# Kernel tuning notes

Measured on AMD Instinct MI355X. Metric: run time of the kernel, lower is better.

Reference implementation:

```python
import jax, jax.numpy as jnp
import numpy as np

N_NODES = 100
F_IN = 65536
C_OUT = 60
ACTION_DIM = 100
N_EDGES = 2000


def setup_inputs() -> dict:
    key = jax.random.key(0)
    ks = jax.random.split(key, 16)
    s = 0.02
    return {
        "substrate_features": jax.random.normal(ks[0], (1, N_NODES, F_IN), jnp.float32),
        "edge_index": jax.random.randint(ks[1], (2, N_EDGES), 0, N_NODES, dtype=jnp.int32),
        "v_cpu_demand_t": jax.random.uniform(ks[2], (1,), jnp.float32),
        "v_bw_demand_t": jax.random.uniform(ks[3], (1,), jnp.float32),
        "num_pending_v_nodes_t": jax.random.uniform(ks[4], (1,), jnp.float32),
        "actor_w": jax.random.normal(ks[5], (3, F_IN, C_OUT), jnp.float32) * s,
        "actor_b": jax.random.normal(ks[6], (C_OUT,), jnp.float32) * s,
        "critic_w": jax.random.normal(ks[7], (3, F_IN, C_OUT), jnp.float32) * s,
        "critic_b": jax.random.normal(ks[8], (C_OUT,), jnp.float32) * s,
        "actor_fc_w": jax.random.normal(ks[9], (N_NODES * C_OUT + 3, ACTION_DIM), jnp.float32) * s,
        "actor_fc_b": jax.random.normal(ks[10], (ACTION_DIM,), jnp.float32) * s,
        "critic_fc_w": jax.random.normal(ks[11], (N_NODES * C_OUT + 3, 1), jnp.float32) * s,
        "critic_fc_b": jax.random.normal(ks[12], (1,), jnp.float32) * s,
    }


def cheb_conv(x, edge_index, W, b):
    # ChebConv, K=3, sym normalization, lambda_max=2 (PyG defaults).
    # With lambda_max=2 the scaled Laplacian is L_hat = -D^{-1/2} A D^{-1/2}
    # (diagonal becomes 0 after the -1 self-loop shift).
    # x: [1, N, F]; edge_index: [2, E]; W: [3, F, C]; b: [C]
    src, dst = edge_index[0], edge_index[1]
    n = x.shape[1]
    deg = jax.ops.segment_sum(jnp.ones(src.shape[0], x.dtype), src, num_segments=n)
    dis = jnp.where(deg > 0, jax.lax.rsqrt(jnp.where(deg > 0, deg, 1.0)), 0.0)
    norm = -(dis[src] * dis[dst])  # [E], L_hat off-diagonal entries
    x2 = x[0]  # [N, F]

    def prop(z):  # z: [N, F] -> L_hat @ z via gather/scatter over edges
        return jax.ops.segment_sum(z[src] * norm[:, None], dst, num_segments=n)

    Tx0 = x2
    Tx1 = prop(Tx0)
    Tx2 = 2.0 * prop(Tx1) - Tx0
    out = Tx0 @ W[0] + Tx1 @ W[1] + Tx2 @ W[2] + b  # [N, C]
    return out[None]  # [1, N, C]


def reference(substrate_features, edge_index, v_cpu_demand_t, v_bw_demand_t,
              num_pending_v_nodes_t, actor_w, actor_b, critic_w, critic_b,
              actor_fc_w, actor_fc_b, critic_fc_w, critic_fc_b):
    emb_a = jnp.tanh(cheb_conv(substrate_features, edge_index, actor_w, actor_b))
    emb_a = emb_a.reshape(1, -1)  # [1, N*60]
    emb_c = jnp.tanh(cheb_conv(substrate_features, edge_index, critic_w, critic_b))
    emb_c = emb_c.reshape(1, -1)
    extras = [v_cpu_demand_t[None], v_bw_demand_t[None], num_pending_v_nodes_t[None]]  # each [1,1]
    state_a = jnp.concatenate([emb_a] + extras, axis=1)  # [1, 6003]
    state_c = jnp.concatenate([emb_c] + extras, axis=1)
    logits = state_a @ actor_fc_w + actor_fc_b  # [1, action_dim]
    values = state_c @ critic_fc_w + critic_fc_b  # [1, 1]
    return (logits, values)
```

## Files before the change

kernel.cpp:

```cpp
#include <hip/hip_runtime.h>
#include <stdint.h>

#define F_IN 65536
#define NN 100
#define CO 60
#define G2 256
#define KC (F_IN/G2)
#define BK 64
#define NIT (KC/BK)
#define AST 72
#define BTILE (BK*CO)
#define BQ3 (3*BTILE/4)

typedef short v8s __attribute__((ext_vector_type(8)));
typedef float v4f __attribute__((ext_vector_type(4)));

__device__ __forceinline__ unsigned int f2bf(float x){
  unsigned int u = __float_as_uint(x);
  u += 0x7fffu + ((u>>16)&1u);
  return u>>16;
}

__device__ __forceinline__ v4f mfma16(v8s a, v8s b, v4f c){
  return __builtin_amdgcn_mfma_f32_16x16x32_bf16(a,b,c,0,0,0);
}

__global__ __launch_bounds__(256,2)
void k_gemm(const float* __restrict__ x, const float* __restrict__ aw,
            const float* __restrict__ cw, float* __restrict__ dst, int partial){
  const int bid  = blockIdx.x;
  const int xcd  = bid & 7, slot = bid >> 3;
  const int net  = slot & 1;
  const int s    = xcd*32 + (slot >> 1);
  const int k0   = s*KC;
  const int tid  = threadIdx.x;
  const int wave = tid>>6, lane = tid&63, quad = lane>>4, nl = lane&15;
  const int c0   = wave*16;
  const int ccl  = min(c0+nl, CO-1);

  const float* Wn = net ? cw : aw;

  __shared__ __align__(16) unsigned short Al[2][112*AST];
  __shared__ __align__(16) unsigned short Bl[2][3*BTILE];

  unsigned int boff[12];
  #pragma unroll
  for(int p=0;p<12;++p){
    int li = min(p*256 + tid, BQ3-1);
    int gp = li/960, fp = li - gp*960;
    boff[p] = (unsigned int)((size_t)gp*F_IN*CO + (size_t)fp*4)*4u;
  }
  const char* bbase0 = (const char*)(Wn + (size_t)k0*CO);

  float4 ra[7];
  float4 rbv[12];
  #pragma unroll
  for(int p=0;p<7;++p){
    int lin = p*256 + tid, row = lin>>4, q = lin&15;
    int rcl = min(row, NN-1);
    ra[p] = *(const float4*)(x + (size_t)rcl*F_IN + k0 + q*4);
  }
  #pragma unroll
  for(int p=0;p<12;++p) rbv[p] = *(const float4*)(bbase0 + boff[p]);

  v4f acc[3][7];
  #pragma unroll
  for(int g=0;g<3;++g)
    #pragma unroll
    for(int i=0;i<7;++i){ v4f z={0.f,0.f,0.f,0.f}; acc[g][i]=z; }

  for(int it=0; it<NIT; ++it){
    unsigned short* buf  = Al[it&1];
    unsigned short* bbuf = Bl[it&1];
    #pragma unroll
    for(int p=0;p<7;++p){
      int lin = p*256 + tid, row = lin>>4, q = lin&15;
      uint2 w;
      w.x = f2bf(ra[p].x) | (f2bf(ra[p].y)<<16);
      w.y = f2bf(ra[p].z) | (f2bf(ra[p].w)<<16);
      *(uint2*)(buf + row*AST + q*4) = w;
    }
    #pragma unroll
    for(int p=0;p<12;++p){
      int lin = p*256 + tid;
      if(lin < BQ3){
        uint2 w;
        w.x = f2bf(rbv[p].x) | (f2bf(rbv[p].y)<<16);
        w.y = f2bf(rbv[p].z) | (f2bf(rbv[p].w)<<16);
        *(uint2*)(bbuf + lin*4) = w;
      }
    }
    __syncthreads();
    if(it+1 < NIT){
      const int kb = k0 + (it+1)*BK;
      #pragma unroll
      for(int p=0;p<7;++p){
        int lin = p*256 + tid, row = lin>>4, q = lin&15;
        int rcl = min(row, NN-1);
        ra[p] = *(const float4*)(x + (size_t)rcl*F_IN + kb + q*4);
      }
      const char* bb2 = bbase0 + (size_t)(it+1)*BK*CO*4;
      #pragma unroll
      for(int p=0;p<12;++p) rbv[p] = *(const float4*)(bb2 + boff[p]);
    }
    __builtin_amdgcn_sched_barrier(0);
    v8s fB0[3], fB1[3];
    #pragma unroll
    for(int g=0;g<3;++g){
      const unsigned short* bb = bbuf + g*BTILE + quad*8*CO + ccl;
      #pragma unroll
      for(int j=0;j<8;++j){
        fB0[g][j] = (short)bb[j*CO];
        fB1[g][j] = (short)bb[32*CO + j*CO];
      }
    }
    #pragma unroll
    for(int mt=0; mt<7; ++mt){
      const unsigned short* arow = buf + (mt*16+nl)*AST + quad*8;
      v8s a0 = *(const v8s*)(arow);
      v8s a1 = *(const v8s*)(arow+32);
      #pragma unroll
      for(int g=0;g<3;++g){
        acc[g][mt] = mfma16(a0, fB0[g], acc[g][mt]);
        acc[g][mt] = mfma16(a1, fB1[g], acc[g][mt]);
      }
    }
  }

  const int c = c0 + nl;
  if(c < CO){
    #pragma unroll
    for(int g=0;g<3;++g){
      if(partial){
        float* pd = dst + ((size_t)(net*3+g)*G2 + s)*(NN*CO);
        #pragma unroll
        for(int mt=0;mt<7;++mt){
          #pragma unroll
          for(int i=0;i<4;++i){
            int m = mt*16 + quad*4 + i;
            if(m < NN) pd[m*CO + c] = acc[g][mt][i];
          }
        }
      } else {
        float* pd = dst + (size_t)(net*3+g)*(NN*CO);
        #pragma unroll
        for(int mt=0;mt<7;++mt){
          #pragma unroll
          for(int i=0;i<4;++i){
            int m = mt*16 + quad*4 + i;
            if(m < NN) atomicAdd(pd + m*CO + c, acc[g][mt][i]);
          }
        }
      }
    }
  }
}

__global__ void k_reduce(const float* __restrict__ P, float* __restrict__ Y){
  int o = blockIdx.x*256 + threadIdx.x;
  if(o >= 6*NN*CO) return;
  int gg = o/(NN*CO), r = o - gg*(NN*CO);
  const float* p = P + (size_t)gg*G2*(NN*CO) + (size_t)blockIdx.y*16*(NN*CO) + r;
  float a0=0.f,a1=0.f,a2=0.f,a3=0.f;
  #pragma unroll
  for(int s4=0;s4<16;s4+=4){
    a0 += p[(size_t)(s4  )*(NN*CO)];
    a1 += p[(size_t)(s4+1)*(NN*CO)];
    a2 += p[(size_t)(s4+2)*(NN*CO)];
    a3 += p[(size_t)(s4+3)*(NN*CO)];
  }
  atomicAdd(&Y[o], (a0+a1)+(a2+a3));
}

__global__ void k_cheb(const float* __restrict__ Y, const int* __restrict__ ei,
                       const float* __restrict__ ab, const float* __restrict__ cb,
                       float* __restrict__ emb, float* __restrict__ out){
  const int net = blockIdx.x / CO;
  const int c   = blockIdx.x % CO;
  const int t   = threadIdx.x;
  __shared__ float L[NN][NN+1];
  __shared__ float dis[NN];
  __shared__ int   deg[NN];
  __shared__ float y0[NN], y1[NN], y2[NN], zu[NN];

  if(blockIdx.x==0 && t<101) out[t] = 0.f;

  for(int i=t;i<NN*(NN+1);i+=128) ((float*)L)[i]=0.f;
  if(t<NN) deg[t]=0;
  __syncthreads();
  for(int e=t;e<2000;e+=128) atomicAdd(&deg[ei[e]],1);
  __syncthreads();
  if(t<NN) dis[t] = deg[t]>0 ? rsqrtf((float)deg[t]) : 0.f;
  __syncthreads();
  for(int e=t;e<2000;e+=128){
    int ss = ei[e], d = ei[2000+e];
    atomicAdd(&L[d][ss], -dis[ss]*dis[d]);
  }
  if(t<NN){
    const float* yb = Y + (size_t)net*3*NN*CO + t*CO + c;
    y0[t]=yb[0]; y1[t]=yb[NN*CO]; y2[t]=yb[2*NN*CO];
  }
  __syncthreads();
  if(t<NN){
    float sv=0.f;
    #pragma unroll 4
    for(int j=0;j<NN;++j) sv += L[t][j]*y2[j];
    zu[t] = y1[t] + 2.f*sv;
  }
  __syncthreads();
  if(t<NN){
    float sv=0.f;
    #pragma unroll 4
    for(int j=0;j<NN;++j) sv += L[t][j]*zu[j];
    float b = (net==0) ? ab[c] : cb[c];
    emb[net*NN*CO + t*CO + c] = tanhf(y0[t] - y2[t] + sv + b);
  }
}

#define FCB 50
__global__ void k_fc(const float* __restrict__ emb, const float* __restrict__ afw,
                     const float* __restrict__ afb, const float* __restrict__ cfw,
                     const float* __restrict__ cfb, const float* __restrict__ s0,
                     const float* __restrict__ s1, const float* __restrict__ s2,
                     float* __restrict__ out){
  const int b = blockIdx.x;
  const int t = threadIdx.x;
  if(b < FCB){
    const int jj = t & 127, half = t >> 7;
    if(jj < 100){
      const int i0 = b*120 + half*60;
      const float* w = afw + (size_t)i0*100 + jj;
      const float* e = emb + i0;
      float p0=0.f,p1=0.f,p2=0.f,p3=0.f;
      #pragma unroll 3
      for(int i=0;i<60;i+=4){
        p0 += e[i  ]*w[(size_t)(i  )*100];
        p1 += e[i+1]*w[(size_t)(i+1)*100];
        p2 += e[i+2]*w[(size_t)(i+2)*100];
        p3 += e[i+3]*w[(size_t)(i+3)*100];
      }
      atomicAdd(&out[jj], (p0+p1)+(p2+p3));
    }
  } else {
    float p = 0.f;
    const float* e = emb + 6000;
    for(int i=t;i<6000;i+=256) p += e[i]*cfw[i];
    #pragma unroll
    for(int o=32;o>0;o>>=1) p += __shfl_down(p,o,64);
    __shared__ float red[4];
    if((t&63)==0) red[t>>6]=p;
    __syncthreads();
    if(t==0){
      float tot = red[0]+red[1]+red[2]+red[3];
      out[100] = tot + s0[0]*cfw[6000] + s1[0]*cfw[6001] + s2[0]*cfw[6002] + cfb[0];
    }
    if(t<100){
      atomicAdd(&out[t], afb[t] + s0[0]*afw[600000+t] + s1[0]*afw[600100+t] + s2[0]*afw[600200+t]);
    }
  }
}

extern "C" void kernel_launch(void* const* d_in, const int* in_sizes, int n_in,
                              void* d_out, int out_size, void* d_ws, size_t ws_size,
                              hipStream_t stream){
  const float* x   = (const float*)d_in[0];
  const int*   ei  = (const int*)d_in[1];
  const float* s0  = (const float*)d_in[2];
  const float* s1  = (const float*)d_in[3];
  const float* s2  = (const float*)d_in[4];
  const float* aw  = (const float*)d_in[5];
  const float* ab  = (const float*)d_in[6];
  const float* cw  = (const float*)d_in[7];
  const float* cb  = (const float*)d_in[8];
  const float* afw = (const float*)d_in[9];
  const float* afb = (const float*)d_in[10];
  const float* cfw = (const float*)d_in[11];
  const float* cfb = (const float*)d_in[12];
  float* out = (float*)d_out;

  float* Y   = (float*)d_ws;
  float* emb = Y + 6*NN*CO;
  float* P   = emb + 2*NN*CO;
  const size_t need = (size_t)(6*NN*CO + 2*NN*CO)*4 + (size_t)6*G2*NN*CO*4;
  const int partial = (ws_size >= need) ? 1 : 0;

  hipMemsetAsync(Y, 0, 6*NN*CO*sizeof(float), stream);

  if(partial){
    k_gemm<<<dim3(512), 256, 0, stream>>>(x, aw, cw, P, 1);
    k_reduce<<<dim3((6*NN*CO+255)/256, 16), 256, 0, stream>>>(P, Y);
  } else {
    k_gemm<<<dim3(512), 256, 0, stream>>>(x, aw, cw, Y, 0);
  }
  k_cheb<<<120, 128, 0, stream>>>(Y, ei, ab, cb, emb, out);
  k_fc<<<FCB+1, 256, 0, stream>>>(emb, afw, afb, cfw, cfb, s0, s1, s2, out);
}
```

Baseline: 238.6 us.

## Load GEMM tiles directly into LDS via global_load_lds and convert to bf16 at read time

```diff
diff --git a/kernel.cpp b/kernel.cpp
--- a/kernel.cpp
+++ b/kernel.cpp
@@ -6,23 +6,32 @@
 #define CO 60
 #define G2 256
 #define KC (F_IN/G2)
-#define BK 64
+#define BK 32
 #define NIT (KC/BK)
-#define AST 72
-#define BTILE (BK*CO)
-#define BQ3 (3*BTILE/4)
+#define ABUF 4096
+#define BBUF 5760
 
 typedef short v8s __attribute__((ext_vector_type(8)));
 typedef float v4f __attribute__((ext_vector_type(4)));
 
-__device__ __forceinline__ unsigned int f2bf(float x){
-  unsigned int u = __float_as_uint(x);
-  u += 0x7fffu + ((u>>16)&1u);
-  return u>>16;
+union U8 { unsigned u[4]; v8s s; };
+
+__device__ __forceinline__ void cvtpk(unsigned &d, float a, float b){
+  asm("v_cvt_pk_bf16_f32 %0, %1, %2" : "=v"(d) : "v"(a), "v"(b));
 }
 
 __device__ __forceinline__ v4f mfma16(v8s a, v8s b, v4f c){
   return __builtin_amdgcn_mfma_f32_16x16x32_bf16(a,b,c,0,0,0);
+}
+
+typedef const __attribute__((address_space(1))) unsigned int* gp_t;
+typedef __attribute__((address_space(3))) unsigned int* lp_t;
+
+__device__ __forceinline__ void gl16(const float* src, float* dst){
+  __builtin_amdgcn_global_load_lds((gp_t)src, (lp_t)dst, 16, 0, 0);
+}
+__device__ __forceinline__ void gl4(const float* src, float* dst){
+  __builtin_amdgcn_global_load_lds((gp_t)src, (lp_t)dst, 4, 0, 0);
 }
 
 __global__ __launch_bounds__(256,2)
@@ -40,28 +49,8 @@
 
   const float* Wn = net ? cw : aw;
 
-  __shared__ __align__(16) unsigned short Al[2][112*AST];
-  __shared__ __align__(16) unsigned short Bl[2][3*BTILE];
-
-  unsigned int boff[12];
-  #pragma unroll
-  for(int p=0;p<12;++p){
-    int li = min(p*256 + tid, BQ3-1);
-    int gp = li/960, fp = li - gp*960;
-    boff[p] = (unsigned int)((size_t)gp*F_IN*CO + (size_t)fp*4)*4u;
-  }
-  const char* bbase0 = (const char*)(Wn + (size_t)k0*CO);
-
-  float4 ra[7];
-  float4 rbv[12];
-  #pragma unroll
-  for(int p=0;p<7;++p){
-    int lin = p*256 + tid, row = lin>>4, q = lin&15;
-    int rcl = min(row, NN-1);
-    ra[p] = *(const float4*)(x + (size_t)rcl*F_IN + k0 + q*4);
-  }
-  #pragma unroll
-  for(int p=0;p<12;++p) rbv[p] = *(const float4*)(bbase0 + boff[p]);
+  __shared__ __align__(16) float Af[2][ABUF];
+  __shared__ __align__(16) float Bf[2][BBUF];
 
   v4f acc[3][7];
   #pragma unroll
@@ -69,61 +58,74 @@
     #pragma unroll
     for(int i=0;i<7;++i){ v4f z={0.f,0.f,0.f,0.f}; acc[g][i]=z; }
 
+  auto stage = [&](float* Afb, float* Bfb, int kb){
+    #pragma unroll
+    for(int p=0;p<4;++p){
+      int j   = wave*4 + p;
+      int w16 = j*64 + lane;
+      int row = w16/9, u = w16 - row*9;
+      int rc  = min(row, NN-1);
+      int uo  = (u==8) ? 0 : u*4;
+      gl16(x + (size_t)rc*F_IN + kb + uo, Afb + j*256);
+    }
+    #pragma unroll
+    for(int p=0;p<7;++p){
+      int idx = p*4 + wave;
+      if(idx < 27){
+        int g = idx/9, t = idx - g*9;
+        const float* WgK = Wn + (size_t)g*F_IN*CO + (size_t)kb*CO;
+        float* dg = Bfb + g*1920;
+        if(t < 7) gl16(WgK + t*256 + lane*4, dg + t*256);
+        else      gl4 (WgK + 1792 + (t-7)*64 + lane, dg + 1792 + (t-7)*64);
+      }
+    }
+  };
+
+  int cur = 0;
+  stage(Af[0], Bf[0], k0);
+  asm volatile("s_waitcnt vmcnt(0)" ::: "memory");
+  __syncthreads();
+
   for(int it=0; it<NIT; ++it){
-    unsigned short* buf  = Al[it&1];
-    unsigned short* bbuf = Bl[it&1];
-    #pragma unroll
-    for(int p=0;p<7;++p){
-      int lin = p*256 + tid, row = lin>>4, q = lin&15;
-      uint2 w;
-      w.x = f2bf(ra[p].x) | (f2bf(ra[p].y)<<16);
-      w.y = f2bf(ra[p].z) | (f2bf(ra[p].w)<<16);
-      *(uint2*)(buf + row*AST + q*4) = w;
-    }
-    #pragma unroll
-    for(int p=0;p<12;++p){
-      int lin = p*256 + tid;
-      if(lin < BQ3){
-        uint2 w;
-        w.x = f2bf(rbv[p].x) | (f2bf(rbv[p].y)<<16);
-        w.y = f2bf(rbv[p].z) | (f2bf(rbv[p].w)<<16);
-        *(uint2*)(bbuf + lin*4) = w;
-      }
-    }
-    __syncthreads();
+    if(it+1 < NIT)
+      stage(Af[cur^1], Bf[cur^1], k0 + (it+1)*BK);
+
+    const float* Afl = Af[cur];
+    const float* Bfl = Bf[cur];
+
+    v8s fB[3];
+    #pragma unroll
+    for(int g=0;g<3;++g){
+      float b0 = Bfl[g*1920 + (quad*8+0)*60 + ccl];
+      float b1 = Bfl[g*1920 + (quad*8+1)*60 + ccl];
+      float b2 = Bfl[g*1920 + (quad*8+2)*60 + ccl];
+      float b3 = Bfl[g*1920 + (quad*8+3)*60 + ccl];
+      float b4 = Bfl[g*1920 + (quad*8+4)*60 + ccl];
+      float b5 = Bfl[g*1920 + (quad*8+5)*60 + ccl];
+      float b6 = Bfl[g*1920 + (quad*8+6)*60 + ccl];
+      float b7 = Bfl[g*1920 + (quad*8+7)*60 + ccl];
+      U8 ub;
+      cvtpk(ub.u[0], b0, b1); cvtpk(ub.u[1], b2, b3);
+      cvtpk(ub.u[2], b4, b5); cvtpk(ub.u[3], b6, b7);
+      fB[g] = ub.s;
+    }
+    #pragma unroll
+    for(int mt=0; mt<7; ++mt){
+      const float* ap = Afl + (mt*16+nl)*36 + quad*8;
+      float4 alo = *(const float4*)(ap);
+      float4 ahi = *(const float4*)(ap+4);
+      U8 ua;
+      cvtpk(ua.u[0], alo.x, alo.y); cvtpk(ua.u[1], alo.z, alo.w);
+      cvtpk(ua.u[2], ahi.x, ahi.y); cvtpk(ua.u[3], ahi.z, ahi.w);
+      #pragma unroll
+      for(int g=0;g<3;++g)
+        acc[g][mt] = mfma16(ua.s, fB[g], acc[g][mt]);
+    }
+
     if(it+1 < NIT){
-      const int kb = k0 + (it+1)*BK;
-      #pragma unroll
-      for(int p=0;p<7;++p){
-        int lin = p*256 + tid, row = lin>>4, q = lin&15;
-        int rcl = min(row, NN-1);
-        ra[p] = *(const float4*)(x + (size_t)rcl*F_IN + kb + q*4);
-      }
-      const char* bb2 = bbase0 + (size_t)(it+1)*BK*CO*4;
-      #pragma unroll
-      for(int p=0;p<12;++p) rbv[p] = *(const float4*)(bb2 + boff[p]);
-    }
-    __builtin_amdgcn_sched_barrier(0);
-    v8s fB0[3], fB1[3];
-    #pragma unroll
-    for(int g=0;g<3;++g){
-      const unsigned short* bb = bbuf + g*BTILE + quad*8*CO + ccl;
-      #pragma unroll
-      for(int j=0;j<8;++j){
-        fB0[g][j] = (short)bb[j*CO];
-        fB1[g][j] = (short)bb[32*CO + j*CO];
-      }
-    }
-    #pragma unroll
-    for(int mt=0; mt<7; ++mt){
-      const unsigned short* arow = buf + (mt*16+nl)*AST + quad*8;
-      v8s a0 = *(const v8s*)(arow);
-      v8s a1 = *(const v8s*)(arow+32);
-      #pragma unroll
-      for(int g=0;g<3;++g){
-        acc[g][mt] = mfma16(a0, fB0[g], acc[g][mt]);
-        acc[g][mt] = mfma16(a1, fB1[g], acc[g][mt]);
-      }
+      asm volatile("s_waitcnt vmcnt(0)" ::: "memory");
+      __syncthreads();
+      cur ^= 1;
     }
   }
 
```

After: 209.9 us. 12.0% less time.
